# Kernel tuning notes

Measured on AMD Instinct MI355X. Metric: run time of the kernel, lower is better.

## Reference

```python
import jax, jax.numpy as jnp
import numpy as np

N = 100000
DEG = 16            # edges per source node (1 self-loop + 15 random)
E = N * DEG
IN_F = 128
OUT_F = 64
ALPHA = 0.2         # leaky relu negative slope


def _build_edges(key):
    # edges sorted by src (as adj.nonzero() would be), every node has >=1 out-edge
    src = jnp.repeat(jnp.arange(N, dtype=jnp.int32), DEG)
    dst = jax.random.randint(key, (E,), 0, N, dtype=jnp.int32)
    # force a self-loop as the first edge of every block
    self_pos = jnp.arange(E, dtype=jnp.int32) % DEG == 0
    dst = jnp.where(self_pos, src, dst)
    return jnp.stack([src, dst])  # [2, E]


def setup_inputs() -> dict:
    key = jax.random.key(0)
    k1, k2, k3, k4, k5, k6 = jax.random.split(key, 6)
    return {
        "input": jax.random.normal(k1, (N, IN_F), dtype=jnp.float32),
        "edge": _build_edges(k2),
        "W_high": jax.random.normal(k3, (IN_F, OUT_F), dtype=jnp.float32) * 0.1,
        "W_low": jax.random.normal(k4, (IN_F, OUT_F), dtype=jnp.float32) * 0.1,
        "a_high": jax.random.normal(k5, (1, 2 * OUT_F), dtype=jnp.float32) * 0.1,
        "a_low": jax.random.normal(k6, (1, 2 * OUT_F), dtype=jnp.float32) * 0.1,
    }


def _relu6(x):
    return jnp.clip(x, 0.0, 6.0)


def reference(input, edge, W_high, W_low, a_high, a_low):
    n = input.shape[0]
    src, dst = edge[0], edge[1]

    h_high = input @ W_high          # [N, F]
    h_low = input @ W_low            # [N, F]

    # a.mm(cat(h[src], h[dst]).T) == (h @ a_src)[src] + (h @ a_dst)[dst]
    f = W_high.shape[1]
    s_high = (h_high @ a_high[0, :f])[src] + (h_high @ a_high[0, f:])[dst]  # [E]
    s_low = (h_low @ a_low[0, :f])[src] + (h_low @ a_low[0, f:])[dst]

    edge_e_high = jnp.exp(-jax.nn.leaky_relu(s_high, ALPHA))  # [E], > 0
    edge_e_low = jnp.exp(-jax.nn.leaky_relu(s_low, ALPHA))

    seg = lambda v: jax.ops.segment_sum(v, src, num_segments=n, indices_are_sorted=True)

    # rowsum uses RAW exp values (before relu6/dropout), matching the source
    e_high_rowsum = seg(edge_e_high)[:, None]  # [N, 1]
    e_low_rowsum = seg(edge_e_low)[:, None]

    # relu6 clamp (dropout p=0 -> identity, eval mode)
    eh = _relu6(edge_e_high)
    el = _relu6(edge_e_low)

    # m @ (h[src] +/- h[dst]) == segment_sum over src of per-edge features
    h_agg_high = seg(h_high[src] + h_high[dst])   # [N, F]
    h_agg_low = seg(h_low[src] - h_low[dst])      # [N, F]

    # spmm: out[i] = sum_{(i,j)} e_ij * h_agg[j]
    h_prime_high = seg(eh[:, None] * h_agg_high[dst]) / e_high_rowsum
    h_prime_low = seg(el[:, None] * h_agg_low[dst]) / e_low_rowsum

    h_prime = 0.5 * (h_prime_high + h_prime_low)
    return _relu6(h_prime)  # concat=True
```

## Files before the change

kernel.cpp:

```cpp
#include <hip/hip_runtime.h>

#define N_NODES 100000
#define DEG 16
#define IN_F 128
#define OUT_F 64
#define E_EDGES (N_NODES * DEG)

typedef __bf16 bf16x8 __attribute__((ext_vector_type(8)));
typedef unsigned short u16x8 __attribute__((ext_vector_type(8)));
typedef float f32x4 __attribute__((ext_vector_type(4)));

union BF8 { u16x8 u; bf16x8 b; };

__device__ inline float lo_bf(unsigned int u) {
    union { unsigned int i; float f; } v; v.i = u << 16; return v.f;
}
__device__ inline float hi_bf(unsigned int u) {
    union { unsigned int i; float f; } v; v.i = u & 0xFFFF0000u; return v.f;
}
__device__ inline unsigned short f2bf(float f) {
    union { float f; unsigned int i; } v; v.f = f;
    return (unsigned short)((v.i + 0x7FFFu + ((v.i >> 16) & 1u)) >> 16);
}
__device__ inline unsigned int packbf(float a, float b) {
    return (unsigned int)f2bf(a) | ((unsigned int)f2bf(b) << 16);
}

__global__ __launch_bounds__(256) void k_gemm(
    const float* __restrict__ in, const float* __restrict__ Wh,
    const float* __restrict__ Wl, unsigned int* __restrict__ H)
{
    __shared__ unsigned short ldsW[2][64][136];
    for (int idx = threadIdx.x; idx < IN_F * OUT_F; idx += 256) {
        int k = idx >> 6, n = idx & 63;
        ldsW[0][n][k] = f2bf(Wh[idx]);
        ldsW[1][n][k] = f2bf(Wl[idx]);
    }
    __syncthreads();

    int wave = blockIdx.x * 4 + (threadIdx.x >> 6);
    int lane = threadIdx.x & 63;
    int row0 = wave * 16;
    if (row0 >= N_NODES) return;

    int quad = lane >> 4, c = lane & 15;
    int mrow = row0 + c;
    int lrow = mrow < N_NODES ? mrow : (N_NODES - 1);

    bf16x8 afrag[4];
    const float* inrow = in + (size_t)lrow * IN_F + quad * 8;
    #pragma unroll
    for (int kb = 0; kb < 4; kb++) {
        f32x4 v0 = *(const f32x4*)(inrow + kb * 32);
        f32x4 v1 = *(const f32x4*)(inrow + kb * 32 + 4);
        bf16x8 a;
        #pragma unroll
        for (int j = 0; j < 4; j++) { a[j] = (__bf16)v0[j]; a[4 + j] = (__bf16)v1[j]; }
        afrag[kb] = a;
    }

    f32x4 acc[2][4];
    #pragma unroll
    for (int m = 0; m < 2; m++)
        #pragma unroll
        for (int t = 0; t < 4; t++) acc[m][t] = (f32x4){0, 0, 0, 0};

    #pragma unroll
    for (int kb = 0; kb < 4; kb++) {
        #pragma unroll
        for (int t = 0; t < 4; t++) {
            int n = t * 16 + c;
            BF8 bh, bl;
            bh.u = *(const u16x8*)&ldsW[0][n][kb * 32 + quad * 8];
            bl.u = *(const u16x8*)&ldsW[1][n][kb * 32 + quad * 8];
            acc[0][t] = __builtin_amdgcn_mfma_f32_16x16x32_bf16(afrag[kb], bh.b, acc[0][t], 0, 0, 0);
            acc[1][t] = __builtin_amdgcn_mfma_f32_16x16x32_bf16(afrag[kb], bl.b, acc[1][t], 0, 0, 0);
        }
    }

    #pragma unroll
    for (int r = 0; r < 4; r++) {
        int row = row0 + quad * 4 + r;
        if (row >= N_NODES) continue;
        size_t base = (size_t)row * OUT_F + c;
        #pragma unroll
        for (int t = 0; t < 4; t++)
            H[base + t * 16] = packbf(acc[0][t][r], acc[1][t][r]);
    }
}

__global__ __launch_bounds__(256) void k_agg(
    const unsigned int* __restrict__ H, const int* __restrict__ dst,
    const float* __restrict__ ah, const float* __restrict__ al,
    unsigned int* __restrict__ HAGG, f32x4* __restrict__ s)
{
    int lane = threadIdx.x & 63;
    int node = __builtin_amdgcn_readfirstlane(blockIdx.x * 4 + (threadIdx.x >> 6));
    const int* dp = dst + node * DEG;

    unsigned int hu = H[(size_t)node * 64 + lane];
    float hh = lo_bf(hu);
    float hl = hi_bf(hu);
    float sh = 16.0f * hh;
    float sl = 16.0f * hl;

    #pragma unroll
    for (int half = 0; half < 2; half++) {
        unsigned int u[8];
        #pragma unroll
        for (int t = 0; t < 8; t++) {
            int j = dp[half * 8 + t];
            u[t] = H[(size_t)j * 64 + lane];
        }
        #pragma unroll
        for (int t = 0; t < 8; t++) { sh += lo_bf(u[t]); sl -= hi_bf(u[t]); }
    }
    HAGG[(size_t)node * 64 + lane] = packbf(sh, sl);

    float ph = hh * ah[lane];
    float qh = hh * ah[64 + lane];
    float pl = hl * al[lane];
    float ql = hl * al[64 + lane];
    #pragma unroll
    for (int o = 32; o > 0; o >>= 1) {
        ph += __shfl_xor(ph, o);
        qh += __shfl_xor(qh, o);
        pl += __shfl_xor(pl, o);
        ql += __shfl_xor(ql, o);
    }
    if (lane == 0) s[node] = (f32x4){ph, qh, pl, ql};
}

__global__ __launch_bounds__(256) void k_out(
    const unsigned int* __restrict__ HAGG, const int* __restrict__ dst,
    const f32x4* __restrict__ s, float* __restrict__ out)
{
    int lane = threadIdx.x & 63;
    int node = __builtin_amdgcn_readfirstlane(blockIdx.x * 4 + (threadIdx.x >> 6));
    const int* dp = dst + node * DEG;

    int jl = dp[lane & 15];
    f32x4 si = s[node];
    f32x4 sj = s[jl];
    float xh = si.x + sj.y;
    float xl = si.z + sj.w;
    float lh = xh > 0.0f ? xh : 0.2f * xh;
    float ll = xl > 0.0f ? xl : 0.2f * xl;
    float wh = __expf(-lh);
    float wl = __expf(-ll);
    float rh = wh, rl = wl;
    #pragma unroll
    for (int o = 8; o > 0; o >>= 1) { rh += __shfl_xor(rh, o); rl += __shfl_xor(rl, o); }
    float eh = fminf(wh, 6.0f);
    float el = fminf(wl, 6.0f);

    float acc_h = 0.0f, acc_l = 0.0f;
    #pragma unroll
    for (int half = 0; half < 2; half++) {
        unsigned int u[8];
        float weh[8], wel[8];
        #pragma unroll
        for (int t = 0; t < 8; t++) {
            int j = dp[half * 8 + t];
            u[t] = HAGG[(size_t)j * 64 + lane];
        }
        #pragma unroll
        for (int t = 0; t < 8; t++) {
            weh[t] = __shfl(eh, half * 8 + t);
            wel[t] = __shfl(el, half * 8 + t);
        }
        #pragma unroll
        for (int t = 0; t < 8; t++) {
            acc_h += weh[t] * lo_bf(u[t]);
            acc_l += wel[t] * hi_bf(u[t]);
        }
    }
    float r = 0.5f * (acc_h / rh + acc_l / rl);
    r = fminf(fmaxf(r, 0.0f), 6.0f);
    out[(size_t)node * 64 + lane] = r;
}

extern "C" void kernel_launch(void* const* d_in, const int* in_sizes, int n_in,
                              void* d_out, int out_size, void* d_ws, size_t ws_size,
                              hipStream_t stream) {
    const float* input = (const float*)d_in[0];
    const int*   edge  = (const int*)d_in[1];
    const float* Wh    = (const float*)d_in[2];
    const float* Wl    = (const float*)d_in[3];
    const float* ah    = (const float*)d_in[4];
    const float* al    = (const float*)d_in[5];
    float* out = (float*)d_out;

    unsigned int* H    = (unsigned int*)d_ws;
    unsigned int* HAGG = H + (size_t)N_NODES * 64;
    f32x4* s = (f32x4*)(HAGG + (size_t)N_NODES * 64);

    const int* dstp = edge + E_EDGES;

    k_gemm<<<1563, 256, 0, stream>>>(input, Wh, Wl, H);
    k_agg<<<N_NODES / 4, 256, 0, stream>>>(H, dstp, ah, al, HAGG, s);
    k_out<<<N_NODES / 4, 256, 0, stream>>>(HAGG, dstp, s, out);
}
```

Measured before the change: 232.6 us.

## Fuse three kernels into one persistent cooperative kernel with grid syncs

Replaces the three separate launches (GEMM, neighbor aggregation, attention spmm) with one cooperative persistent kernel. The grid is sized from occupancy times CU count, each phase loops over its tiles or nodes, and phases are separated by grid.sync. This targets launch gaps and per-kernel tail effects, but it adds occupancy and device-attribute queries on the host for every call, limits each block to 256 threads at occupancy hint 2, and introduces grid-wide barrier costs. The old three-kernel path is kept as a fallback.

```diff
diff --git a/kernel.cpp b/kernel.cpp
--- a/kernel.cpp
+++ b/kernel.cpp
@@ -1,10 +1,15 @@
 #include <hip/hip_runtime.h>
+#include <hip/hip_cooperative_groups.h>
+
+namespace cg = cooperative_groups;
 
 #define N_NODES 100000
 #define DEG 16
 #define IN_F 128
 #define OUT_F 64
 #define E_EDGES (N_NODES * DEG)
+#define NTILES 1563
+#define NQUADS 25000
 
 typedef __bf16 bf16x8 __attribute__((ext_vector_type(8)));
 typedef unsigned short u16x8 __attribute__((ext_vector_type(8)));
@@ -24,6 +29,166 @@
 }
 __device__ inline unsigned int packbf(float a, float b) {
     return (unsigned int)f2bf(a) | ((unsigned int)f2bf(b) << 16);
+}
+
+__global__ __launch_bounds__(256, 2) void k_fused(
+    const float* __restrict__ in, const float* __restrict__ Wh,
+    const float* __restrict__ Wl, const int* __restrict__ dst,
+    const float* __restrict__ ah, const float* __restrict__ al,
+    unsigned int* __restrict__ H, unsigned int* __restrict__ HAGG,
+    f32x4* __restrict__ s, float* __restrict__ out)
+{
+    cg::grid_group grid = cg::this_grid();
+    __shared__ unsigned short ldsW[2][64][136];
+
+    int wv = threadIdx.x >> 6;
+    int lane = threadIdx.x & 63;
+    int quad = lane >> 4, c = lane & 15;
+    int nblk = gridDim.x;
+
+    for (int idx = threadIdx.x; idx < IN_F * OUT_F; idx += 256) {
+        int k = idx >> 6, n = idx & 63;
+        ldsW[0][n][k] = f2bf(Wh[idx]);
+        ldsW[1][n][k] = f2bf(Wl[idx]);
+    }
+    __syncthreads();
+
+    for (int tile = blockIdx.x; tile < NTILES; tile += nblk) {
+        int row0 = tile * 64 + wv * 16;
+        int mrow = row0 + c;
+        int lrow = mrow < N_NODES ? mrow : (N_NODES - 1);
+
+        bf16x8 afrag[4];
+        const float* inrow = in + (size_t)lrow * IN_F + quad * 8;
+        #pragma unroll
+        for (int kb = 0; kb < 4; kb++) {
+            f32x4 v0 = *(const f32x4*)(inrow + kb * 32);
+            f32x4 v1 = *(const f32x4*)(inrow + kb * 32 + 4);
+            bf16x8 a;
+            #pragma unroll
+            for (int j = 0; j < 4; j++) { a[j] = (__bf16)v0[j]; a[4 + j] = (__bf16)v1[j]; }
+            afrag[kb] = a;
+        }
+
+        f32x4 acc[2][4];
+        #pragma unroll
+        for (int m = 0; m < 2; m++)
+            #pragma unroll
+            for (int t = 0; t < 4; t++) acc[m][t] = (f32x4){0, 0, 0, 0};
+
+        #pragma unroll
+        for (int kb = 0; kb < 4; kb++) {
+            #pragma unroll
+            for (int t = 0; t < 4; t++) {
+                int n = t * 16 + c;
+                BF8 bh, bl;
+                bh.u = *(const u16x8*)&ldsW[0][n][kb * 32 + quad * 8];
+                bl.u = *(const u16x8*)&ldsW[1][n][kb * 32 + quad * 8];
+                acc[0][t] = __builtin_amdgcn_mfma_f32_16x16x32_bf16(afrag[kb], bh.b, acc[0][t], 0, 0, 0);
+                acc[1][t] = __builtin_amdgcn_mfma_f32_16x16x32_bf16(afrag[kb], bl.b, acc[1][t], 0, 0, 0);
+            }
+        }
+
+        #pragma unroll
+        for (int r = 0; r < 4; r++) {
+            int row = row0 + quad * 4 + r;
+            if (row >= N_NODES) continue;
+            size_t base = (size_t)row * OUT_F + c;
+            #pragma unroll
+            for (int t = 0; t < 4; t++)
+                H[base + t * 16] = packbf(acc[0][t][r], acc[1][t][r]);
+        }
+    }
+
+    __threadfence();
+    grid.sync();
+    __threadfence();
+
+    for (int q = blockIdx.x; q < NQUADS; q += nblk) {
+        int node = __builtin_amdgcn_readfirstlane(q * 4 + wv);
+        const int* dp = dst + node * DEG;
+
+        unsigned int hu = H[(size_t)node * 64 + lane];
+        float hh = lo_bf(hu);
+        float hl = hi_bf(hu);
+        float sh = 16.0f * hh;
+        float sl = 16.0f * hl;
+
+        #pragma unroll
+        for (int half = 0; half < 2; half++) {
+            unsigned int u[8];
+            #pragma unroll
+            for (int t = 0; t < 8; t++) {
+                int j = dp[half * 8 + t];
+                u[t] = H[(size_t)j * 64 + lane];
+            }
+            #pragma unroll
+            for (int t = 0; t < 8; t++) { sh += lo_bf(u[t]); sl -= hi_bf(u[t]); }
+        }
+        HAGG[(size_t)node * 64 + lane] = packbf(sh, sl);
+
+        float ph = hh * ah[lane];
+        float qh = hh * ah[64 + lane];
+        float pl = hl * al[lane];
+        float ql = hl * al[64 + lane];
+        #pragma unroll
+        for (int o = 32; o > 0; o >>= 1) {
+            ph += __shfl_xor(ph, o);
+            qh += __shfl_xor(qh, o);
+            pl += __shfl_xor(pl, o);
+            ql += __shfl_xor(ql, o);
+        }
+        if (lane == 0) s[node] = (f32x4){ph, qh, pl, ql};
+    }
+
+    __threadfence();
+    grid.sync();
+    __threadfence();
+
+    for (int q = blockIdx.x; q < NQUADS; q += nblk) {
+        int node = __builtin_amdgcn_readfirstlane(q * 4 + wv);
+        const int* dp = dst + node * DEG;
+
+        int jl = dp[lane & 15];
+        f32x4 si = s[node];
+        f32x4 sj = s[jl];
+        float xh = si.x + sj.y;
+        float xl = si.z + sj.w;
+        float lh = xh > 0.0f ? xh : 0.2f * xh;
+        float ll = xl > 0.0f ? xl : 0.2f * xl;
+        float wh = __expf(-lh);
+        float wl = __expf(-ll);
+        float rh = wh, rl = wl;
+        #pragma unroll
+        for (int o = 8; o > 0; o >>= 1) { rh += __shfl_xor(rh, o); rl += __shfl_xor(rl, o); }
+        float eh = fminf(wh, 6.0f);
+        float el = fminf(wl, 6.0f);
+
+        float acc_h = 0.0f, acc_l = 0.0f;
+        #pragma unroll
+        for (int half = 0; half < 2; half++) {
+            unsigned int u[8];
+            float weh[8], wel[8];
+            #pragma unroll
+            for (int t = 0; t < 8; t++) {
+                int j = dp[half * 8 + t];
+                u[t] = HAGG[(size_t)j * 64 + lane];
+            }
+            #pragma unroll
+            for (int t = 0; t < 8; t++) {
+                weh[t] = __shfl(eh, half * 8 + t);
+                wel[t] = __shfl(el, half * 8 + t);
+            }
+            #pragma unroll
+            for (int t = 0; t < 8; t++) {
+                acc_h += weh[t] * lo_bf(u[t]);
+                acc_l += wel[t] * hi_bf(u[t]);
+            }
+        }
+        float r = 0.5f * (acc_h / rh + acc_l / rl);
+        r = fminf(fmaxf(r, 0.0f), 6.0f);
+        out[(size_t)node * 64 + lane] = r;
+    }
 }
 
 __global__ __launch_bounds__(256) void k_gemm(
@@ -42,7 +207,6 @@
     int lane = threadIdx.x & 63;
     int row0 = wave * 16;
     if (row0 >= N_NODES) return;
-
     int quad = lane >> 4, c = lane & 15;
     int mrow = row0 + c;
     int lrow = mrow < N_NODES ? mrow : (N_NODES - 1);
@@ -197,7 +361,26 @@
 
     const int* dstp = edge + E_EDGES;
 
-    k_gemm<<<1563, 256, 0, stream>>>(input, Wh, Wl, H);
-    k_agg<<<N_NODES / 4, 256, 0, stream>>>(H, dstp, ah, al, HAGG, s);
-    k_out<<<N_NODES / 4, 256, 0, stream>>>(HAGG, dstp, s, out);
-}
+    int occ = 0, ncu = 0;
+    hipError_t e1 = hipOccupancyMaxActiveBlocksPerMultiprocessor(
+        &occ, (const void*)k_fused, 256, 0);
+    hipError_t e2 = hipDeviceGetAttribute(&ncu, hipDeviceAttributeMultiprocessorCount, 0);
+    bool launched = false;
+    if (e1 == hipSuccess && e2 == hipSuccess && occ > 0 && ncu > 0) {
+        int blks = occ * ncu;
+        if (blks > NTILES) blks = NTILES;
+        void* args[] = {
+            (void*)&input, (void*)&Wh, (void*)&Wl, (void*)&dstp,
+            (void*)&ah, (void*)&al, (void*)&H, (void*)&HAGG,
+            (void*)&s, (void*)&out
+        };
+        hipError_t le = hipLaunchCooperativeKernel((const void*)k_fused, dim3(blks),
+                                                   dim3(256), args, 0, stream);
+        launched = (le == hipSuccess);
+    }
+    if (!launched) {
+        k_gemm<<<1563, 256, 0, stream>>>(input, Wh, Wl, H);
+        k_agg<<<NQUADS, 256, 0, stream>>>(H, dstp, ah, al, HAGG, s);
+        k_out<<<NQUADS, 256, 0, stream>>>(HAGG, dstp, s, out);
+    }
+}
```

New measurement: 507.1 us. +118.0%, slower.
